# Optimization experiments

Measured on AMD Instinct MI355X. Metric: run time of the kernel, lower is better.

Reference implementation:

```python
import jax, jax.numpy as jnp
import numpy as np

N = 50000      # total nodes
E = 500000     # edges
D = 128        # in_channels
B = 50         # graphs in batch
NPG = N // B   # nodes per graph (equal-sized graphs)
RATIO = 0.5
ALPHA = 0.6


def setup_inputs() -> dict:
    key = jax.random.key(0)
    ks = jax.random.split(key, 8)
    x = jax.random.normal(ks[0], (N, D), dtype=jnp.float32)
    edge_index = jax.random.randint(ks[1], (2, E), 0, N, dtype=jnp.int32)
    batch = jnp.repeat(jnp.arange(B, dtype=jnp.int32), NPG)  # sorted, equal blocks
    s = 1.0 / np.sqrt(D)
    # GCNConv(D,1) for structure score
    W_s = jax.random.normal(ks[2], (D, 1), dtype=jnp.float32) * s
    b_s = jnp.zeros((1,), dtype=jnp.float32)
    # Linear(D,1) for feature score
    W_f = jax.random.normal(ks[3], (1, D), dtype=jnp.float32) * s
    b_f = jnp.zeros((1,), dtype=jnp.float32)
    # GCNConv(D,D) fusion layer
    W_fu = jax.random.normal(ks[4], (D, D), dtype=jnp.float32) * s
    b_fu = jnp.zeros((D,), dtype=jnp.float32)
    return {"x": x, "edge_index": edge_index, "batch": batch,
            "W_s": W_s, "b_s": b_s, "W_f": W_f, "b_f": b_f,
            "W_fu": W_fu, "b_fu": b_fu}


def gcn_conv(x, src, dst, W, b, n):
    """PyG GCNConv: add self loops, symmetric D^-1/2 (A+I) D^-1/2 @ (xW) + b."""
    xw = x @ W                                  # [n, out]
    loop = jnp.arange(n, dtype=src.dtype)
    s = jnp.concatenate([src, loop])
    d = jnp.concatenate([dst, loop])
    deg = jax.ops.segment_sum(jnp.ones_like(s, dtype=xw.dtype), d, num_segments=n)
    dinv = jax.lax.rsqrt(jnp.maximum(deg, 1e-12))
    norm = dinv[s] * dinv[d]                    # [E+n]
    out = jax.ops.segment_sum(norm[:, None] * xw[s], d, num_segments=n)
    return out + b


def reference(x, edge_index, batch, W_s, b_s, W_f, b_f, W_fu, b_fu):
    src, dst = edge_index[0], edge_index[1]
    # fused score: alpha * structure (GCN) + (1-alpha) * feature (Linear)
    score_s = gcn_conv(x, src, dst, W_s, b_s, N)[:, 0]          # [N]
    score_f = (x @ W_f.T + b_f)[:, 0]                           # [N]
    score = jnp.tanh(ALPHA * score_s + (1.0 - ALPHA) * score_f)
    # per-graph top-k (equal-sized graphs -> dense [B, NPG] view, like the torch topk)
    k = int(np.ceil(RATIO * NPG))
    dense = score.reshape(B, NPG)
    order = jnp.argsort(-dense, axis=-1)                        # descending
    offsets = (jnp.arange(B, dtype=jnp.int32) * NPG)[:, None]
    perm = (order[:, :k].astype(jnp.int32) + offsets).reshape(-1)  # [B*k]
    # fusion conv on full graph, then gather selected nodes
    x_fused = gcn_conv(x, src, dst, W_fu, b_fu, N)              # [N, D]
    x_ae = x_fused[perm]                                        # [B*k, D]
    x_out = x_ae * score[perm][:, None]                         # multiplier == 1
    batch_out = batch[perm]
    # filter_adj: remap node ids, keep edges with both endpoints selected
    nodemap = jnp.full((N,), -1, dtype=jnp.int32).at[perm].set(
        jnp.arange(perm.shape[0], dtype=jnp.int32))
    r, c = nodemap[src], nodemap[dst]
    m = (r >= 0) & (c >= 0)
    edge_index_new = jnp.stack([r[m], c[m]], axis=0)
    return (x_out, edge_index_new, batch_out, perm, x_ae)
```

## Files before the change

kernel.cpp:

```cpp
#include <hip/hip_runtime.h>
#include <math.h>

#define N_NODES 50000
#define N_EDGES 500000
#define DIM     128
#define NGRAPH  50
#define NPGC    1000
#define KSEL    500
#define SORT_N  1024
#define NBE     489
#define NBN     49
#define GEMM_BLKS 782
#define DEG_BLKS  1954
#define DOTS_BLKS 12500
#define NDINV     196
#define GATH_BLKS 6250


__global__ __launch_bounds__(256) void k1_gemm_deg(const float* __restrict__ x,
                                                   const float* __restrict__ W,
                                                   float* __restrict__ xw,
                                                   const int* __restrict__ dst,
                                                   int* __restrict__ deg) {
    __shared__ float lds[12288];
    int t = threadIdx.x;
    if (blockIdx.x >= GEMM_BLKS) {
        int e = (blockIdx.x - GEMM_BLKS) * 256 + t;
        if (e < N_EDGES) atomicAdd(&deg[dst[e]], 1);
        return;
    }
    float* Wt = lds;
    float* Xt = lds + 64 * DIM;
    int cg = t & 15;
    int ng = t >> 4;
    int node_base = blockIdx.x * 64;

    float4 acc[4][2];
    #pragma unroll
    for (int nn = 0; nn < 4; nn++) {
        acc[nn][0] = make_float4(0.f, 0.f, 0.f, 0.f);
        acc[nn][1] = make_float4(0.f, 0.f, 0.f, 0.f);
    }
    for (int half = 0; half < 2; half++) {
        const float4* Wg = (const float4*)(W + half * 64 * DIM);
        float4* Wl = (float4*)Wt;
        #pragma unroll
        for (int i = 0; i < 8; i++) {
            int f = t + i * 256;
            Wl[f] = Wg[f];
        }
        #pragma unroll
        for (int i = 0; i < 4; i++) {
            int f = t + i * 256;
            int row = f >> 4, col = f & 15;
            int node = node_base + row;
            float4 v = make_float4(0.f, 0.f, 0.f, 0.f);
            if (node < N_NODES) v = *(const float4*)&x[(size_t)node * DIM + half * 64 + col * 4];
            *(float4*)&Xt[(row << 6) + ((col ^ (row & 15)) << 2)] = v;
        }
        __syncthreads();
        #pragma unroll 2
        for (int kc = 0; kc < 16; kc++) {
            int k = kc << 2;
            float4 wa[4], wb[4];
            #pragma unroll
            for (int kk = 0; kk < 4; kk++) {
                wa[kk] = *(const float4*)&Wt[(k + kk) * DIM + (cg << 2)];
                wb[kk] = *(const float4*)&Wt[(k + kk) * DIM + (cg << 2) + 64];
            }
            int csw = (kc ^ ng) << 2;
            #pragma unroll
            for (int nn = 0; nn < 4; nn++) {
                float4 xv = *(const float4*)&Xt[((ng + (nn << 4)) << 6) + csw];
                acc[nn][0].x += xv.x * wa[0].x + xv.y * wa[1].x + xv.z * wa[2].x + xv.w * wa[3].x;
                acc[nn][0].y += xv.x * wa[0].y + xv.y * wa[1].y + xv.z * wa[2].y + xv.w * wa[3].y;
                acc[nn][0].z += xv.x * wa[0].z + xv.y * wa[1].z + xv.z * wa[2].z + xv.w * wa[3].z;
                acc[nn][0].w += xv.x * wa[0].w + xv.y * wa[1].w + xv.z * wa[2].w + xv.w * wa[3].w;
                acc[nn][1].x += xv.x * wb[0].x + xv.y * wb[1].x + xv.z * wb[2].x + xv.w * wb[3].x;
                acc[nn][1].y += xv.x * wb[0].y + xv.y * wb[1].y + xv.z * wb[2].y + xv.w * wb[3].y;
                acc[nn][1].z += xv.x * wb[0].z + xv.y * wb[1].z + xv.z * wb[2].z + xv.w * wb[3].z;
                acc[nn][1].w += xv.x * wb[0].w + xv.y * wb[1].w + xv.z * wb[2].w + xv.w * wb[3].w;
            }
        }
        __syncthreads();
    }
    #pragma unroll
    for (int nn = 0; nn < 4; nn++) {
        int node = node_base + ng + (nn << 4);
        if (node < N_NODES) {
            *(float4*)&xw[(size_t)node * DIM + (cg << 2)]      = acc[nn][0];
            *(float4*)&xw[(size_t)node * DIM + (cg << 2) + 64] = acc[nn][1];
        }
    }
}


__global__ __launch_bounds__(256) void k2_dots_scan_dinv(const int* __restrict__ deg,
                                                         int* __restrict__ rowoff,
                                                         int* __restrict__ bsumsN,
                                                         const float* __restrict__ x,
                                                         const float* __restrict__ Ws,
                                                         const float* __restrict__ Wf,
                                                         const float* __restrict__ bf,
                                                         double* __restrict__ pack,
                                                         float* __restrict__ dinvf,
                                                         double* __restrict__ sf) {
    int t = threadIdx.x;
    int lane = t & 63, wid = t >> 6;
    int bid = blockIdx.x;
    if (bid < DOTS_BLKS) {
        int node = bid * 4 + wid;
        const float* xr = x + (size_t)node * DIM;
        double x1 = (double)xr[lane], x2 = (double)xr[lane + 64];
        double ps = x1 * (double)Ws[lane] + x2 * (double)Ws[lane + 64];
        double pf = x1 * (double)Wf[lane] + x2 * (double)Wf[lane + 64];
        for (int off = 32; off > 0; off >>= 1) {
            ps += __shfl_down(ps, off, 64);
            pf += __shfl_down(pf, off, 64);
        }
        if (lane == 0) {
            pack[2 * node + 1] = ps;
            sf[node] = pf + (double)bf[0];
        }
        return;
    }
    if (bid < DOTS_BLKS + NBN) {
        __shared__ int ws4[4];
        int base = (bid - DOTS_BLKS) * 1024 + t * 4;
        int v0 = (base + 0 < N_NODES) ? deg[base + 0] : 0;
        int v1 = (base + 1 < N_NODES) ? deg[base + 1] : 0;
        int v2 = (base + 2 < N_NODES) ? deg[base + 2] : 0;
        int v3 = (base + 3 < N_NODES) ? deg[base + 3] : 0;
        int s4 = v0 + v1 + v2 + v3;
        int incl = s4;
        #pragma unroll
        for (int off = 1; off < 64; off <<= 1) {
            int u = __shfl_up(incl, off, 64);
            if (lane >= off) incl += u;
        }
        if (lane == 63) ws4[wid] = incl;
        __syncthreads();
        int woff = 0;
        #pragma unroll
        for (int w = 0; w < 4; w++) if (w < wid) woff += ws4[w];
        int excl = incl - s4 + woff;
        if (base + 0 < N_NODES) rowoff[base + 0] = excl;
        if (base + 1 < N_NODES) rowoff[base + 1] = excl + v0;
        if (base + 2 < N_NODES) rowoff[base + 2] = excl + v0 + v1;
        if (base + 3 < N_NODES) rowoff[base + 3] = excl + v0 + v1 + v2;
        if (t == 255) bsumsN[bid - DOTS_BLKS] = woff + incl;
        return;
    }
    int i = (bid - DOTS_BLKS - NBN) * 256 + t;
    if (i < N_NODES) {
        double di = 1.0 / sqrt((double)(deg[i] + 1));
        pack[2 * i] = di;
        dinvf[i] = (float)di;
    }
}


__global__ __launch_bounds__(256) void k3_csr(const int* __restrict__ src,
                                              const int* __restrict__ dst,
                                              const int* __restrict__ rowoff,
                                              const int* __restrict__ bsumsN,
                                              int* __restrict__ cursor,
                                              int* __restrict__ csr) {
    __shared__ int bsN[64];
    int t = threadIdx.x;
    if (t < 64) {
        int v = (t < NBN) ? bsumsN[t] : 0;
        int incl = v;
        #pragma unroll
        for (int off = 1; off < 64; off <<= 1) {
            int u = __shfl_up(incl, off, 64);
            if (t >= off) incl += u;
        }
        bsN[t] = incl - v;
    }
    __syncthreads();
    int e = blockIdx.x * 256 + t;
    if (e >= N_EDGES) return;
    int d = dst[e];
    int pos = rowoff[d] + bsN[d >> 10] + atomicAdd(&cursor[d], 1);
    csr[pos] = src[e];
}


__global__ __launch_bounds__(256) void k3b_score(const int* __restrict__ csr,
                                                 const int* __restrict__ rowoff,
                                                 const int* __restrict__ bsumsN,
                                                 const int* __restrict__ deg,
                                                 const double* __restrict__ pack,
                                                 double* __restrict__ score_sd) {
    __shared__ int bsN[64];
    int t = threadIdx.x;
    if (t < 64) {
        int v = (t < NBN) ? bsumsN[t] : 0;
        int incl = v;
        #pragma unroll
        for (int off = 1; off < 64; off <<= 1) {
            int u = __shfl_up(incl, off, 64);
            if (t >= off) incl += u;
        }
        bsN[t] = incl - v;
    }
    __syncthreads();
    int node = blockIdx.x * 256 + t;
    if (node >= N_NODES) return;
    int base = rowoff[node] + bsN[node >> 10];
    int cnt  = deg[node];
    double acc0 = 0.0, acc1 = 0.0;
    int i = 0;
    for (; i + 2 <= cnt; i += 2) {
        int s0 = csr[base + i];
        int s1 = csr[base + i + 1];
        double2 p0 = ((const double2*)pack)[s0];
        double2 p1 = ((const double2*)pack)[s1];
        acc0 += p0.x * p0.y;
        acc1 += p1.x * p1.y;
    }
    if (i < cnt) {
        int s0 = csr[base + i];
        double2 p0 = ((const double2*)pack)[s0];
        acc0 += p0.x * p0.y;
    }
    score_sd[node] = pack[2 * node] * (acc0 + acc1);
}


__global__ __launch_bounds__(512) void k4_topk(const double* __restrict__ score_sd,
                                               const double* __restrict__ pack,
                                               const double* __restrict__ sf,
                                               const float* __restrict__ bs,
                                               const int* __restrict__ batch,
                                               int* __restrict__ perm, int* __restrict__ nodemap,
                                               float* __restrict__ scoref_sel,
                                               float* __restrict__ out, long o2, long o3) {
    __shared__ double key[SORT_N];
    __shared__ int    idx[SORT_N];
    int g = blockIdx.x, t = threadIdx.x;
    const double A = 0.6, OMA = 1.0 - 0.6;
    double bsv = (double)bs[0];
    for (int i = t; i < SORT_N; i += 512) {
        if (i < NPGC) {
            int node = g * NPGC + i;
            double2 p = ((const double2*)pack)[node];
            double tot = score_sd[node] + p.x * p.x * p.y + bsv;
            key[i] = tanh(A * tot + OMA * sf[node]);
            idx[i] = i;
        } else { key[i] = -1e300; idx[i] = i; }
    }
    __syncthreads();
    for (int size = 2; size <= SORT_N; size <<= 1) {
        for (int stride = size >> 1; stride > 0; stride >>= 1) {
            int a = ((t & ~(stride - 1)) << 1) | (t & (stride - 1));
            int b = a | stride;
            bool descFirst = ((a & size) == 0);
            double ka = key[a], kb = key[b];
            int ia = idx[a], ib = idx[b];
            bool aAfterB = (ka < kb) || (ka == kb && ia > ib);
            if (descFirst ? aAfterB : !aAfterB) {
                key[a] = kb; key[b] = ka;
                idx[a] = ib; idx[b] = ia;
            }
            __syncthreads();
        }
    }
    for (int j = t; j < KSEL; j += 512) {
        int node = g * NPGC + idx[j];
        int pos  = g * KSEL + j;
        perm[pos]        = node;
        nodemap[node]    = pos + 1;
        scoref_sel[pos]  = (float)key[j];
        out[o2 + pos]    = (float)batch[node];
        out[o3 + pos]    = (float)node;
    }
}


__global__ __launch_bounds__(256) void k5_escan_gather(const int* __restrict__ src,
                                                       const int* __restrict__ dst,
                                                       const int* __restrict__ nodemap,
                                                       int* __restrict__ epos,
                                                       int* __restrict__ bsumsE,
                                                       const float* __restrict__ xw,
                                                       const int* __restrict__ perm,
                                                       const int* __restrict__ rowoff,
                                                       const int* __restrict__ bsumsN,
                                                       const int* __restrict__ deg,
                                                       const int* __restrict__ csr,
                                                       const float* __restrict__ dinvf,
                                                       const float* __restrict__ scoref_sel,
                                                       const float* __restrict__ b_fu,
                                                       float* __restrict__ out, long o4) {
    int t = threadIdx.x;
    int lane = t & 63, wid = t >> 6;
    if (blockIdx.x < NBE) {
        __shared__ int ws4[4];
        int base = blockIdx.x * 1024 + t * 4;
        int v0 = 0, v1 = 0, v2 = 0, v3 = 0;
        if (base + 0 < N_EDGES) v0 = (nodemap[src[base + 0]] > 0 && nodemap[dst[base + 0]] > 0);
        if (base + 1 < N_EDGES) v1 = (nodemap[src[base + 1]] > 0 && nodemap[dst[base + 1]] > 0);
        if (base + 2 < N_EDGES) v2 = (nodemap[src[base + 2]] > 0 && nodemap[dst[base + 2]] > 0);
        if (base + 3 < N_EDGES) v3 = (nodemap[src[base + 3]] > 0 && nodemap[dst[base + 3]] > 0);
        int s4 = v0 + v1 + v2 + v3;
        int incl = s4;
        #pragma unroll
        for (int off = 1; off < 64; off <<= 1) {
            int u = __shfl_up(incl, off, 64);
            if (lane >= off) incl += u;
        }
        if (lane == 63) ws4[wid] = incl;
        __syncthreads();
        int woff = 0;
        #pragma unroll
        for (int w = 0; w < 4; w++) if (w < wid) woff += ws4[w];
        int excl = incl - s4 + woff;
        if (base + 0 < N_EDGES) epos[base + 0] = excl;
        if (base + 1 < N_EDGES) epos[base + 1] = excl + v0;
        if (base + 2 < N_EDGES) epos[base + 2] = excl + v0 + v1;
        if (base + 3 < N_EDGES) epos[base + 3] = excl + v0 + v1 + v2;
        if (t == 255) bsumsE[blockIdx.x] = woff + incl;
        return;
    }
    __shared__ int bsN[64];
    if (t < 64) {
        int v = (t < NBN) ? bsumsN[t] : 0;
        int incl = v;
        #pragma unroll
        for (int off = 1; off < 64; off <<= 1) {
            int u = __shfl_up(incl, off, 64);
            if (t >= off) incl += u;
        }
        bsN[t] = incl - v;
    }
    __syncthreads();
    int wave = (blockIdx.x - NBE) * 4 + wid;
    int p = perm[wave];
    float dpf = dinvf[p];
    int c2 = lane * 2;
    float2 v = ((const float2*)(xw + (size_t)p * DIM))[lane];
    float nself = dpf * dpf;
    float ax = nself * v.x, ay = nself * v.y;
    int beg = rowoff[p] + bsN[p >> 10], cnt = deg[p];
    int i = 0;
    for (; i + 2 <= cnt; i += 2) {
        int s0 = csr[beg + i];
        int s1 = csr[beg + i + 1];
        float2 u0 = ((const float2*)(xw + (size_t)s0 * DIM))[lane];
        float2 u1 = ((const float2*)(xw + (size_t)s1 * DIM))[lane];
        float n0 = dinvf[s0] * dpf, n1 = dinvf[s1] * dpf;
        ax += n0 * u0.x; ay += n0 * u0.y;
        ax += n1 * u1.x; ay += n1 * u1.y;
    }
    if (i < cnt) {
        int s0 = csr[beg + i];
        float2 u0 = ((const float2*)(xw + (size_t)s0 * DIM))[lane];
        float n0 = dinvf[s0] * dpf;
        ax += n0 * u0.x; ay += n0 * u0.y;
    }
    ax += b_fu[c2];
    ay += b_fu[c2 + 1];
    float sc = scoref_sel[wave];
    size_t ro = (size_t)wave * DIM + c2;
    out[o4 + ro]     = ax;
    out[o4 + ro + 1] = ay;
    out[ro]          = ax * sc;
    out[ro + 1]      = ay * sc;
}


__global__ __launch_bounds__(256) void k6_compact(const int* __restrict__ src,
                                                  const int* __restrict__ dst,
                                                  const int* __restrict__ nodemap,
                                                  const int* __restrict__ epos,
                                                  const int* __restrict__ bsumsE,
                                                  float* __restrict__ out_edges, long M) {
    __shared__ int bsE[512];
    int t = threadIdx.x;
    if (t < 64) {
        int carry = 0;
        #pragma unroll
        for (int c = 0; c < 8; c++) {
            int i = c * 64 + t;
            int v = (i < NBE) ? bsumsE[i] : 0;
            int incl = v;
            #pragma unroll
            for (int off = 1; off < 64; off <<= 1) {
                int u = __shfl_up(incl, off, 64);
                if (t >= off) incl += u;
            }
            if (i < 512) bsE[i] = incl - v + carry;
            carry += __shfl(incl, 63, 64);
        }
    }
    __syncthreads();
    int e = blockIdx.x * 256 + t;
    if (e >= N_EDGES) return;
    int r = nodemap[src[e]], c = nodemap[dst[e]];
    if (r > 0 && c > 0) {
        int pos = epos[e] + bsE[e >> 10];
        out_edges[pos]     = (float)(r - 1);
        out_edges[M + pos] = (float)(c - 1);
    }
}


extern "C" void kernel_launch(void* const* d_in, const int* in_sizes, int n_in,
                              void* d_out, int out_size, void* d_ws, size_t ws_size,
                              hipStream_t stream) {
    const float* x    = (const float*)d_in[0];
    const int*   ei   = (const int*)d_in[1];
    const int*   src  = ei;
    const int*   dst  = ei + N_EDGES;
    const int*   batch= (const int*)d_in[2];
    const float* W_s  = (const float*)d_in[3];
    const float* b_s  = (const float*)d_in[4];
    const float* W_f  = (const float*)d_in[5];
    const float* b_f  = (const float*)d_in[6];
    const float* W_fu = (const float*)d_in[7];
    const float* b_fu = (const float*)d_in[8];
    float* out = (float*)d_out;

    char* wsp = (char*)d_ws;
    size_t off = 0;
    auto take = [&](size_t bytes) -> char* {
        char* p = wsp + off;
        off = (off + bytes + 255) & ~(size_t)255;
        return p;
    };
    char*   zbase      = wsp;
    int*    deg        = (int*)   take((size_t)N_NODES * 4);
    int*    cursor     = (int*)   take((size_t)N_NODES * 4);
    int*    nodemap    = (int*)   take((size_t)N_NODES * 4);
    size_t  zbytes     = off;
    double* score_sd   = (double*)take((size_t)N_NODES * 8);
    double* pack       = (double*)take((size_t)N_NODES * 16);
    double* sf         = (double*)take((size_t)N_NODES * 8);
    float*  dinvf      = (float*) take((size_t)N_NODES * 4);
    float*  scoref_sel = (float*) take((size_t)NGRAPH * KSEL * 4);
    int*    perm       = (int*)   take((size_t)NGRAPH * KSEL * 4);
    int*    rowoff     = (int*)   take((size_t)N_NODES * 4);
    int*    epos       = (int*)   take((size_t)N_EDGES * 4);
    int*    bsumsE     = (int*)   take((size_t)1024 * 4);
    int*    bsumsN     = (int*)   take((size_t)1024 * 4);
    int*    csr        = (int*)   take((size_t)N_EDGES * 4);
    float*  xw         = (float*) take((size_t)N_NODES * DIM * 4);

    long M  = ((long)out_size - 6450000L) / 2;
    long o1 = 3200000L;
    long o2 = o1 + 2 * M;
    long o3 = o2 + (long)NGRAPH * KSEL;
    long o4 = o3 + (long)NGRAPH * KSEL;

    hipMemsetAsync(zbase, 0, zbytes, stream);

    k1_gemm_deg<<<GEMM_BLKS + DEG_BLKS, 256, 0, stream>>>(x, W_fu, xw, dst, deg);
    k2_dots_scan_dinv<<<DOTS_BLKS + NBN + NDINV, 256, 0, stream>>>(deg, rowoff, bsumsN,
                                                                   x, W_s, W_f, b_f,
                                                                   pack, dinvf, sf);
    k3_csr<<<DEG_BLKS, 256, 0, stream>>>(src, dst, rowoff, bsumsN, cursor, csr);
    k3b_score<<<NDINV, 256, 0, stream>>>(csr, rowoff, bsumsN, deg, pack, score_sd);
    k4_topk<<<NGRAPH, 512, 0, stream>>>(score_sd, pack, sf, b_s, batch,
                                        perm, nodemap, scoref_sel, out, o2, o3);
    k5_escan_gather<<<NBE + GATH_BLKS, 256, 0, stream>>>(src, dst, nodemap, epos, bsumsE,
                                                         xw, perm, rowoff, bsumsN, deg, csr,
                                                         dinvf, scoref_sel, b_fu, out, o4);
    k6_compact<<<DEG_BLKS, 256, 0, stream>>>(src, dst, nodemap, epos, bsumsE, out + o1, M);
}
```

Baseline: 237.1 us.

## Record edge slots from degree atomics and replicate counters to drop CSR cursor atomics

The degree-count pass now spreads atomics over 8 replicated counter arrays, chosen by edge index. It stores each edge's returned slot and replica id in a new per-edge array. The dinv pass turns the replicated counts into per-replica offsets and a total degree. The CSR fill then computes each edge's position directly instead of doing a second atomic per edge on a cursor array. This removes one full pass of atomics and lowers counter contention, at the cost of a larger memset, an extra per-edge read and write, and 8x more reads in the degree scan.

```diff
diff --git a/kernel.cpp b/kernel.cpp
--- a/kernel.cpp
+++ b/kernel.cpp
@@ -15,18 +15,25 @@
 #define DOTS_BLKS 12500
 #define NDINV     196
 #define GATH_BLKS 6250
+#define NREP    8
 
 
 __global__ __launch_bounds__(256) void k1_gemm_deg(const float* __restrict__ x,
                                                    const float* __restrict__ W,
                                                    float* __restrict__ xw,
                                                    const int* __restrict__ dst,
-                                                   int* __restrict__ deg) {
+                                                   int* __restrict__ degrep,
+                                                   int* __restrict__ eslot) {
     __shared__ float lds[12288];
     int t = threadIdx.x;
     if (blockIdx.x >= GEMM_BLKS) {
         int e = (blockIdx.x - GEMM_BLKS) * 256 + t;
-        if (e < N_EDGES) atomicAdd(&deg[dst[e]], 1);
+        if (e < N_EDGES) {
+            int d = dst[e];
+            int r = e & (NREP - 1);
+            int old = atomicAdd(&degrep[r * N_NODES + d], 1);
+            eslot[e] = (old << 3) | r;
+        }
         return;
     }
     float* Wt = lds;
@@ -95,7 +102,9 @@
 }
 
 
-__global__ __launch_bounds__(256) void k2_dots_scan_dinv(const int* __restrict__ deg,
+__global__ __launch_bounds__(256) void k2_dots_scan_dinv(const int* __restrict__ degrep,
+                                                         int* __restrict__ repoff,
+                                                         int* __restrict__ deg,
                                                          int* __restrict__ rowoff,
                                                          int* __restrict__ bsumsN,
                                                          const float* __restrict__ x,
@@ -127,10 +136,14 @@
     if (bid < DOTS_BLKS + NBN) {
         __shared__ int ws4[4];
         int base = (bid - DOTS_BLKS) * 1024 + t * 4;
-        int v0 = (base + 0 < N_NODES) ? deg[base + 0] : 0;
-        int v1 = (base + 1 < N_NODES) ? deg[base + 1] : 0;
-        int v2 = (base + 2 < N_NODES) ? deg[base + 2] : 0;
-        int v3 = (base + 3 < N_NODES) ? deg[base + 3] : 0;
+        int v0 = 0, v1 = 0, v2 = 0, v3 = 0;
+        if (base < N_NODES) {
+            #pragma unroll
+            for (int r = 0; r < NREP; r++) {
+                int4 vv = *(const int4*)&degrep[r * N_NODES + base];
+                v0 += vv.x; v1 += vv.y; v2 += vv.z; v3 += vv.w;
+            }
+        }
         int s4 = v0 + v1 + v2 + v3;
         int incl = s4;
         #pragma unroll
@@ -153,7 +166,15 @@
     }
     int i = (bid - DOTS_BLKS - NBN) * 256 + t;
     if (i < N_NODES) {
-        double di = 1.0 / sqrt((double)(deg[i] + 1));
+        int o = 0;
+        #pragma unroll
+        for (int r = 0; r < NREP; r++) {
+            int c = degrep[r * N_NODES + i];
+            repoff[r * N_NODES + i] = o;
+            o += c;
+        }
+        deg[i] = o;
+        double di = 1.0 / sqrt((double)(o + 1));
         pack[2 * i] = di;
         dinvf[i] = (float)di;
     }
@@ -164,7 +185,8 @@
                                               const int* __restrict__ dst,
                                               const int* __restrict__ rowoff,
                                               const int* __restrict__ bsumsN,
-                                              int* __restrict__ cursor,
+                                              const int* __restrict__ repoff,
+                                              const int* __restrict__ eslot,
                                               int* __restrict__ csr) {
     __shared__ int bsN[64];
     int t = threadIdx.x;
@@ -182,7 +204,9 @@
     int e = blockIdx.x * 256 + t;
     if (e >= N_EDGES) return;
     int d = dst[e];
-    int pos = rowoff[d] + bsN[d >> 10] + atomicAdd(&cursor[d], 1);
+    int es = eslot[e];
+    int r = es & (NREP - 1), slot = es >> 3;
+    int pos = rowoff[d] + bsN[d >> 10] + repoff[r * N_NODES + d] + slot;
     csr[pos] = src[e];
 }
 
@@ -431,10 +455,12 @@
         return p;
     };
     char*   zbase      = wsp;
-    int*    deg        = (int*)   take((size_t)N_NODES * 4);
-    int*    cursor     = (int*)   take((size_t)N_NODES * 4);
+    int*    degrep     = (int*)   take((size_t)NREP * N_NODES * 4);
     int*    nodemap    = (int*)   take((size_t)N_NODES * 4);
     size_t  zbytes     = off;
+    int*    repoff     = (int*)   take((size_t)NREP * N_NODES * 4);
+    int*    eslot      = (int*)   take((size_t)N_EDGES * 4);
+    int*    deg        = (int*)   take((size_t)N_NODES * 4);
     double* score_sd   = (double*)take((size_t)N_NODES * 8);
     double* pack       = (double*)take((size_t)N_NODES * 16);
     double* sf         = (double*)take((size_t)N_NODES * 8);
@@ -456,11 +482,12 @@
 
     hipMemsetAsync(zbase, 0, zbytes, stream);
 
-    k1_gemm_deg<<<GEMM_BLKS + DEG_BLKS, 256, 0, stream>>>(x, W_fu, xw, dst, deg);
-    k2_dots_scan_dinv<<<DOTS_BLKS + NBN + NDINV, 256, 0, stream>>>(deg, rowoff, bsumsN,
+    k1_gemm_deg<<<GEMM_BLKS + DEG_BLKS, 256, 0, stream>>>(x, W_fu, xw, dst, degrep, eslot);
+    k2_dots_scan_dinv<<<DOTS_BLKS + NBN + NDINV, 256, 0, stream>>>(degrep, repoff, deg,
+                                                                   rowoff, bsumsN,
                                                                    x, W_s, W_f, b_f,
                                                                    pack, dinvf, sf);
-    k3_csr<<<DEG_BLKS, 256, 0, stream>>>(src, dst, rowoff, bsumsN, cursor, csr);
+    k3_csr<<<DEG_BLKS, 256, 0, stream>>>(src, dst, rowoff, bsumsN, repoff, eslot, csr);
     k3b_score<<<NDINV, 256, 0, stream>>>(csr, rowoff, bsumsN, deg, pack, score_sd);
     k4_topk<<<NGRAPH, 512, 0, stream>>>(score_sd, pack, sf, b_s, batch,
                                         perm, nodemap, scoref_sel, out, o2, o3);
```

New measurement: 220.9 us. -6.9%, faster.
